# Kernel optimization log

Measured on AMD Instinct MI355X. Metric: run time of the kernel, lower is better.

Reference implementation:

```python
import jax, jax.numpy as jnp
import numpy as np

B, V = 256, 128000

def setup_inputs() -> dict:
    key = jax.random.key(0)
    k1, k2, k3 = jax.random.split(key, 3)
    logits = jax.random.normal(k1, (B, V), dtype=jnp.float32)
    # temperatures in [0,1); force a few exact zeros to exercise the greedy path
    temperatures = jax.random.uniform(k2, (B,), dtype=jnp.float32)
    temperatures = temperatures.at[:8].set(0.0)
    # uniform noise for Gumbel-max sampling (stand-in for torch.multinomial RNG)
    uniform_noise = jax.random.uniform(k3, (B, V), dtype=jnp.float32,
                                       minval=1e-7, maxval=1.0 - 1e-7)
    return {"logits": logits, "temperatures": temperatures, "uniform_noise": uniform_noise}

def reference(logits, temperatures, uniform_noise):
    logits = logits.astype(jnp.float32)
    greedy_tokens = jnp.argmax(logits, axis=-1)                     # [B]
    safe_t = jnp.where(temperatures == 0, jnp.ones_like(temperatures), temperatures)
    scaled = logits / safe_t[:, None]                               # [B, V]
    probs = jax.nn.softmax(scaled, axis=-1)                         # [B, V]
    # Gumbel-max trick: argmax(scaled + g), g ~ Gumbel(0,1) == multinomial(probs)
    gumbel = -jnp.log(-jnp.log(uniform_noise))
    sample_tokens = jnp.argmax(scaled + gumbel, axis=-1)            # [B]
    tokens = jnp.where(temperatures == 0, greedy_tokens, sample_tokens)
    return tokens, probs
```

## Files before the change

kernel.cpp:

```cpp
#include <hip/hip_runtime.h>
#include <math.h>

#define BATCH 256
#define VOCAB 128000
#define V4 (VOCAB / 4)
#define NTHREADS 1024
#define NWAVES (NTHREADS / 64)

typedef float vfloat4 __attribute__((ext_vector_type(4)));

__global__ __launch_bounds__(NTHREADS) void sampler_kernel(
    const float* __restrict__ logits,
    const float* __restrict__ temps,
    const float* __restrict__ noise,
    float* __restrict__ out_tokens,
    float* __restrict__ out_probs)
{
    const int b    = blockIdx.x;
    const int tid  = threadIdx.x;
    const int wave = tid >> 6;
    const int lane = tid & 63;

    const float t      = temps[b];
    const float safe_t = (t == 0.0f) ? 1.0f : t;
    const float inv_t  = 1.0f / safe_t;

    const vfloat4* lg4 = (const vfloat4*)(logits + (size_t)b * VOCAB);
    const vfloat4* nz4 = (const vfloat4*)(noise  + (size_t)b * VOCAB);
    vfloat4*       pb4 = (vfloat4*)(out_probs + (size_t)b * VOCAB);

    float gv0 = -INFINITY, gv1 = -INFINITY;
    int   gi0 = 0,          gi1 = 0;
    float s0  = 0.0f,       s1  = 0.0f;
    float sv0 = -INFINITY,  sv1 = -INFINITY;
    int   si0 = 0,          si1 = 0;

    auto proc1 = [&](const vfloat4 x4, const vfloat4 u4, int idx0,
                     float& gv, int& gi, float& s, float& sv, int& si) {
        float v01 = fmaxf(x4[0], x4[1]);
        int   i01 = (x4[1] > x4[0]) ? idx0 + 1 : idx0;
        float v23 = fmaxf(x4[2], x4[3]);
        int   i23 = (x4[3] > x4[2]) ? idx0 + 3 : idx0 + 2;
        float cm  = fmaxf(v01, v23);
        int   cmi = (v23 > v01) ? i23 : i01;

        float e0 = __expf((x4[0] - cm) * inv_t);
        float e1 = __expf((x4[1] - cm) * inv_t);
        float e2 = __expf((x4[2] - cm) * inv_t);
        float e3 = __expf((x4[3] - cm) * inv_t);
        float cs = (e0 + e1) + (e2 + e3);

        float mn = fmaxf(gv, cm);
        s = s * __expf((gv - mn) * inv_t) + cs * __expf((cm - mn) * inv_t);
        if (cm > gv) gi = cmi;
        gv = mn;

        float g0 = -__logf(-__logf(u4[0]));
        float g1 = -__logf(-__logf(u4[1]));
        float g2 = -__logf(-__logf(u4[2]));
        float g3 = -__logf(-__logf(u4[3]));
        float z0 = x4[0] * inv_t + g0;
        float z1 = x4[1] * inv_t + g1;
        float z2 = x4[2] * inv_t + g2;
        float z3 = x4[3] * inv_t + g3;
        float w01 = fmaxf(z0, z1);
        int   j01 = (z1 > z0) ? idx0 + 1 : idx0;
        float w23 = fmaxf(z2, z3);
        int   j23 = (z3 > z2) ? idx0 + 3 : idx0 + 2;
        float wm  = fmaxf(w01, w23);
        int   wmi = (w23 > w01) ? j23 : j01;
        if (wm > sv) { si = wmi; sv = wm; }
    };

    int i = tid;
    for (; i + NTHREADS < V4; i += 2 * NTHREADS) {
        vfloat4 xa = lg4[i];
        vfloat4 xb = lg4[i + NTHREADS];
        vfloat4 ua = __builtin_nontemporal_load(&nz4[i]);
        vfloat4 ub = __builtin_nontemporal_load(&nz4[i + NTHREADS]);
        proc1(xa, ua, 4 * i,              gv0, gi0, s0, sv0, si0);
        proc1(xb, ub, 4 * (i + NTHREADS), gv1, gi1, s1, sv1, si1);
    }
    if (i < V4) {
        vfloat4 xa = lg4[i];
        vfloat4 ua = __builtin_nontemporal_load(&nz4[i]);
        proc1(xa, ua, 4 * i, gv0, gi0, s0, sv0, si0);
    }

    {
        float mn = fmaxf(gv0, gv1);
        s0 = s0 * __expf((gv0 - mn) * inv_t) + s1 * __expf((gv1 - mn) * inv_t);
        if (gv1 > gv0 || (gv1 == gv0 && gi1 < gi0)) gi0 = gi1;
        gv0 = mn;
        if (sv1 > sv0 || (sv1 == sv0 && si1 < si0)) { sv0 = sv1; si0 = si1; }
    }

#pragma unroll
    for (int off = 32; off >= 1; off >>= 1) {
        float gv2 = __shfl_down(gv0, off);
        int   gi2 = __shfl_down(gi0, off);
        float s2  = __shfl_down(s0,  off);
        float sv2 = __shfl_down(sv0, off);
        int   si2 = __shfl_down(si0, off);
        float mn = fmaxf(gv0, gv2);
        s0 = s0 * __expf((gv0 - mn) * inv_t) + s2 * __expf((gv2 - mn) * inv_t);
        if (gv2 > gv0 || (gv2 == gv0 && gi2 < gi0)) gi0 = gi2;
        gv0 = mn;
        if (sv2 > sv0 || (sv2 == sv0 && si2 < si0)) { sv0 = sv2; si0 = si2; }
    }

    __shared__ float sh_gv[NWAVES], sh_s[NWAVES], sh_sv[NWAVES];
    __shared__ int   sh_gi[NWAVES], sh_si[NWAVES];
    __shared__ float bGV, binvS;
    if (lane == 0) {
        sh_gv[wave] = gv0; sh_s[wave] = s0; sh_gi[wave] = gi0;
        sh_sv[wave] = sv0; sh_si[wave] = si0;
    }
    __syncthreads();
    if (tid == 0) {
        float GVr = sh_gv[0], S = sh_s[0], SV = sh_sv[0];
        int   GI  = sh_gi[0], SI = sh_si[0];
        for (int w = 1; w < NWAVES; ++w) {
            float mn = fmaxf(GVr, sh_gv[w]);
            S = S * __expf((GVr - mn) * inv_t) + sh_s[w] * __expf((sh_gv[w] - mn) * inv_t);
            if (sh_gv[w] > GVr || (sh_gv[w] == GVr && sh_gi[w] < GI)) GI = sh_gi[w];
            GVr = mn;
            if (sh_sv[w] > SV || (sh_sv[w] == SV && sh_si[w] < SI)) { SV = sh_sv[w]; SI = sh_si[w]; }
        }
        bGV = GVr; binvS = 1.0f / S;
        out_tokens[b] = (float)((t == 0.0f) ? GI : SI);
    }
    __syncthreads();
    const float Msc  = bGV * inv_t;
    const float invS = binvS;

    int k = tid;
    for (; k + NTHREADS < V4; k += 2 * NTHREADS) {
        vfloat4 xa = lg4[k];
        vfloat4 xb = lg4[k + NTHREADS];
        vfloat4 pa, pb;
#pragma unroll
        for (int j = 0; j < 4; ++j)
            pa[j] = __expf(fmaf(xa[j], inv_t, -Msc)) * invS;
#pragma unroll
        for (int j = 0; j < 4; ++j)
            pb[j] = __expf(fmaf(xb[j], inv_t, -Msc)) * invS;
        __builtin_nontemporal_store(pa, &pb4[k]);
        __builtin_nontemporal_store(pb, &pb4[k + NTHREADS]);
    }
    if (k < V4) {
        vfloat4 xa = lg4[k];
        vfloat4 pa;
#pragma unroll
        for (int j = 0; j < 4; ++j)
            pa[j] = __expf(fmaf(xa[j], inv_t, -Msc)) * invS;
        __builtin_nontemporal_store(pa, &pb4[k]);
    }
}

extern "C" void kernel_launch(void* const* d_in, const int* in_sizes, int n_in,
                              void* d_out, int out_size, void* d_ws, size_t ws_size,
                              hipStream_t stream) {
    const float* logits = (const float*)d_in[0];
    const float* temps  = (const float*)d_in[1];
    const float* noise  = (const float*)d_in[2];
    float* out = (float*)d_out;
    sampler_kernel<<<BATCH, NTHREADS, 0, stream>>>(logits, temps, noise,
                                                   out, out + BATCH);
}
```

Measured before the change: 321.9 us.

## Launch two blocks per row, each redoing reduction and writing half of probs

Doubles the grid so each batch row is handled by two blocks. Both blocks redundantly compute the full max/sum/argmax pass, and each writes only half of the probability output. This aims to raise occupancy across the CUs, since 256 blocks underfill the device. In exchange it doubles the reads of logits and noise in the reduction pass. It also drops the two-accumulator unroll and uses a branchy online-softmax update.

Result: no change. 324.2 us (+0.7%).

```diff
diff --git a/kernel.cpp b/kernel.cpp
--- a/kernel.cpp
+++ b/kernel.cpp
@@ -4,7 +4,9 @@
 #define BATCH 256
 #define VOCAB 128000
 #define V4 (VOCAB / 4)
+#define V2_4 (V4 / 2)
 #define NTHREADS 1024
+#define NT NTHREADS
 #define NWAVES (NTHREADS / 64)
 
 typedef float vfloat4 __attribute__((ext_vector_type(4)));
@@ -16,7 +18,12 @@
     float* __restrict__ out_tokens,
     float* __restrict__ out_probs)
 {
-    const int b    = blockIdx.x;
+    const int p    = blockIdx.x;
+    const int j    = p & 7;
+    const int half = (p >> 3) & 1;
+    const int k    = p >> 4;
+    const int b    = k * 8 + j;
+
     const int tid  = threadIdx.x;
     const int wave = tid >> 6;
     const int lane = tid & 63;
@@ -29,14 +36,14 @@
     const vfloat4* nz4 = (const vfloat4*)(noise  + (size_t)b * VOCAB);
     vfloat4*       pb4 = (vfloat4*)(out_probs + (size_t)b * VOCAB);
 
-    float gv0 = -INFINITY, gv1 = -INFINITY;
-    int   gi0 = 0,          gi1 = 0;
-    float s0  = 0.0f,       s1  = 0.0f;
-    float sv0 = -INFINITY,  sv1 = -INFINITY;
-    int   si0 = 0,          si1 = 0;
+    float gv = -INFINITY, s = 0.0f, sv = -INFINITY;
+    int   gi = 0, si = 0;
 
-    auto proc1 = [&](const vfloat4 x4, const vfloat4 u4, int idx0,
-                     float& gv, int& gi, float& s, float& sv, int& si) {
+    for (int i = tid; i < V4; i += NT) {
+        vfloat4 x4 = lg4[i];
+        vfloat4 u4 = __builtin_nontemporal_load(&nz4[i]);
+        const int idx0 = 4 * i;
+
         float v01 = fmaxf(x4[0], x4[1]);
         int   i01 = (x4[1] > x4[0]) ? idx0 + 1 : idx0;
         float v23 = fmaxf(x4[2], x4[3]);
@@ -50,10 +57,12 @@
         float e3 = __expf((x4[3] - cm) * inv_t);
         float cs = (e0 + e1) + (e2 + e3);
 
-        float mn = fmaxf(gv, cm);
-        s = s * __expf((gv - mn) * inv_t) + cs * __expf((cm - mn) * inv_t);
-        if (cm > gv) gi = cmi;
-        gv = mn;
+        if (cm > gv) {
+            s = s * __expf((gv - cm) * inv_t) + cs;
+            gv = cm; gi = cmi;
+        } else {
+            s += cs * __expf((cm - gv) * inv_t);
+        }
 
         float g0 = -__logf(-__logf(u4[0]));
         float g1 = -__logf(-__logf(u4[1]));
@@ -70,91 +79,57 @@
         float wm  = fmaxf(w01, w23);
         int   wmi = (w23 > w01) ? j23 : j01;
         if (wm > sv) { si = wmi; sv = wm; }
-    };
-
-    int i = tid;
-    for (; i + NTHREADS < V4; i += 2 * NTHREADS) {
-        vfloat4 xa = lg4[i];
-        vfloat4 xb = lg4[i + NTHREADS];
-        vfloat4 ua = __builtin_nontemporal_load(&nz4[i]);
-        vfloat4 ub = __builtin_nontemporal_load(&nz4[i + NTHREADS]);
-        proc1(xa, ua, 4 * i,              gv0, gi0, s0, sv0, si0);
-        proc1(xb, ub, 4 * (i + NTHREADS), gv1, gi1, s1, sv1, si1);
-    }
-    if (i < V4) {
-        vfloat4 xa = lg4[i];
-        vfloat4 ua = __builtin_nontemporal_load(&nz4[i]);
-        proc1(xa, ua, 4 * i, gv0, gi0, s0, sv0, si0);
-    }
-
-    {
-        float mn = fmaxf(gv0, gv1);
-        s0 = s0 * __expf((gv0 - mn) * inv_t) + s1 * __expf((gv1 - mn) * inv_t);
-        if (gv1 > gv0 || (gv1 == gv0 && gi1 < gi0)) gi0 = gi1;
-        gv0 = mn;
-        if (sv1 > sv0 || (sv1 == sv0 && si1 < si0)) { sv0 = sv1; si0 = si1; }
     }
 
 #pragma unroll
     for (int off = 32; off >= 1; off >>= 1) {
-        float gv2 = __shfl_down(gv0, off);
-        int   gi2 = __shfl_down(gi0, off);
-        float s2  = __shfl_down(s0,  off);
-        float sv2 = __shfl_down(sv0, off);
-        int   si2 = __shfl_down(si0, off);
-        float mn = fmaxf(gv0, gv2);
-        s0 = s0 * __expf((gv0 - mn) * inv_t) + s2 * __expf((gv2 - mn) * inv_t);
-        if (gv2 > gv0 || (gv2 == gv0 && gi2 < gi0)) gi0 = gi2;
-        gv0 = mn;
-        if (sv2 > sv0 || (sv2 == sv0 && si2 < si0)) { sv0 = sv2; si0 = si2; }
+        float gv2 = __shfl_down(gv, off);
+        int   gi2 = __shfl_down(gi, off);
+        float s2  = __shfl_down(s,  off);
+        float sv2 = __shfl_down(sv, off);
+        int   si2 = __shfl_down(si, off);
+        float mn = fmaxf(gv, gv2);
+        s = s * __expf((gv - mn) * inv_t) + s2 * __expf((gv2 - mn) * inv_t);
+        if (gv2 > gv || (gv2 == gv && gi2 < gi)) gi = gi2;
+        gv = mn;
+        if (sv2 > sv || (sv2 == sv && si2 < si)) { sv = sv2; si = si2; }
     }
 
     __shared__ float sh_gv[NWAVES], sh_s[NWAVES], sh_sv[NWAVES];
     __shared__ int   sh_gi[NWAVES], sh_si[NWAVES];
     __shared__ float bGV, binvS;
     if (lane == 0) {
-        sh_gv[wave] = gv0; sh_s[wave] = s0; sh_gi[wave] = gi0;
-        sh_sv[wave] = sv0; sh_si[wave] = si0;
+        sh_gv[wave] = gv; sh_s[wave] = s; sh_gi[wave] = gi;
+        sh_sv[wave] = sv; sh_si[wave] = si;
     }
     __syncthreads();
     if (tid == 0) {
-        float GVr = sh_gv[0], S = sh_s[0], SV = sh_sv[0];
-        int   GI  = sh_gi[0], SI = sh_si[0];
+        float GV = sh_gv[0], S = sh_s[0], SV = sh_sv[0];
+        int   GI = sh_gi[0], SI = sh_si[0];
         for (int w = 1; w < NWAVES; ++w) {
-            float mn = fmaxf(GVr, sh_gv[w]);
-            S = S * __expf((GVr - mn) * inv_t) + sh_s[w] * __expf((sh_gv[w] - mn) * inv_t);
-            if (sh_gv[w] > GVr || (sh_gv[w] == GVr && sh_gi[w] < GI)) GI = sh_gi[w];
-            GVr = mn;
+            float mn = fmaxf(GV, sh_gv[w]);
+            S = S * __expf((GV - mn) * inv_t) + sh_s[w] * __expf((sh_gv[w] - mn) * inv_t);
+            if (sh_gv[w] > GV || (sh_gv[w] == GV && sh_gi[w] < GI)) GI = sh_gi[w];
+            GV = mn;
             if (sh_sv[w] > SV || (sh_sv[w] == SV && sh_si[w] < SI)) { SV = sh_sv[w]; SI = sh_si[w]; }
         }
-        bGV = GVr; binvS = 1.0f / S;
-        out_tokens[b] = (float)((t == 0.0f) ? GI : SI);
+        bGV = GV; binvS = 1.0f / S;
+        if (half == 0)
+            out_tokens[b] = (float)((t == 0.0f) ? GI : SI);
     }
     __syncthreads();
     const float Msc  = bGV * inv_t;
     const float invS = binvS;
 
-    int k = tid;
-    for (; k + NTHREADS < V4; k += 2 * NTHREADS) {
-        vfloat4 xa = lg4[k];
-        vfloat4 xb = lg4[k + NTHREADS];
-        vfloat4 pa, pb;
+    const vfloat4* lgh = lg4 + half * V2_4;
+    vfloat4*       pbh = pb4 + half * V2_4;
+    for (int i = tid; i < V2_4; i += NT) {
+        vfloat4 x4 = lgh[i];
+        vfloat4 pr;
 #pragma unroll
-        for (int j = 0; j < 4; ++j)
-            pa[j] = __expf(fmaf(xa[j], inv_t, -Msc)) * invS;
-#pragma unroll
-        for (int j = 0; j < 4; ++j)
-            pb[j] = __expf(fmaf(xb[j], inv_t, -Msc)) * invS;
-        __builtin_nontemporal_store(pa, &pb4[k]);
-        __builtin_nontemporal_store(pb, &pb4[k + NTHREADS]);
-    }
-    if (k < V4) {
-        vfloat4 xa = lg4[k];
-        vfloat4 pa;
-#pragma unroll
-        for (int j = 0; j < 4; ++j)
-            pa[j] = __expf(fmaf(xa[j], inv_t, -Msc)) * invS;
-        __builtin_nontemporal_store(pa, &pb4[k]);
+        for (int jj = 0; jj < 4; ++jj)
+            pr[jj] = __expf(fmaf(x4[jj], inv_t, -Msc)) * invS;
+        __builtin_nontemporal_store(pr, &pbh[i]);
     }
 }
 
@@ -165,6 +140,6 @@
     const float* temps  = (const float*)d_in[1];
     const float* noise  = (const float*)d_in[2];
     float* out = (float*)d_out;
-    sampler_kernel<<<BATCH, NTHREADS, 0, stream>>>(logits, temps, noise,
-                                                   out, out + BATCH);
+    sampler_kernel<<<BATCH * 2, NTHREADS, 0, stream>>>(logits, temps, noise,
+                                                       out, out + BATCH);
 }
```
